# Performance work log

Measured on AMD Instinct MI355X. Metric: run time of the kernel, lower is better.

Reference implementation:

```python
import jax, jax.numpy as jnp
import numpy as np

N = 50000      # num nodes (spots)
E = 800000     # num edges before self-loops
IN = 3000      # input_dim (HVGs)
HID = 512      # hidden_dim
LAT = 30       # latent_dim
HEADS = 1
NEG_SLOPE = 0.2


def setup_inputs() -> dict:
    key = jax.random.key(0)
    ks = jax.random.split(key, 8)
    x = jax.random.normal(ks[0], (N, IN), jnp.float32)
    edge_index = jax.random.randint(ks[1], (2, E), 0, N)
    edge_attr = jax.random.uniform(ks[2], (E,), jnp.float32)
    # parameters (Xavier-ish scales)
    enc_w1 = jax.random.normal(ks[3], (HID, IN), jnp.float32) * (1.0 / np.sqrt(IN))
    enc_b1 = jnp.zeros((HID,), jnp.float32)
    gat_w = jax.random.normal(ks[4], (HID, HEADS * LAT), jnp.float32) * (1.0 / np.sqrt(HID))
    gat_att = jax.random.normal(ks[5], (HEADS, 2 * LAT), jnp.float32) * 0.1
    gat_b = jnp.zeros((LAT,), jnp.float32)
    dec_w1 = jax.random.normal(ks[6], (HID, LAT), jnp.float32) * (1.0 / np.sqrt(LAT))
    dec_b1 = jnp.zeros((HID,), jnp.float32)
    dec_b2 = jnp.zeros((IN,), jnp.float32)
    return dict(x=x, edge_index=edge_index, edge_attr=edge_attr,
                enc_w1=enc_w1, enc_b1=enc_b1, gat_w=gat_w, gat_att=gat_att,
                gat_b=gat_b, dec_w1=dec_w1, dec_b1=dec_b1, dec_b2=dec_b2)


def _gat_layer(h, src, dst, eattr, gat_w, gat_att, gat_b):
    """GAT layer: Eq.5-7, concat=False (mean over heads), multiplicative edge_attr."""
    xh = (h @ gat_w).reshape(N, HEADS, LAT)          # W h, per head
    x_i = xh[dst]                                     # target node feats (E+N, H, LAT)
    x_j = xh[src]                                     # source node feats
    att_i, att_j = gat_att[:, :LAT], gat_att[:, LAT:]
    # e_ij = LeakyReLU(a^T [Wh_i || Wh_j])
    alpha = jnp.einsum('ehc,hc->eh', x_i, att_i) + jnp.einsum('ehc,hc->eh', x_j, att_j)
    alpha = jax.nn.leaky_relu(alpha, NEG_SLOPE)
    alpha = alpha * eattr[:, None]                    # edge weight applied pre-softmax
    # segment softmax over incoming edges of each target node (self-loops ensure non-empty)
    amax = jax.ops.segment_max(alpha, dst, num_segments=N)
    alpha = jnp.exp(alpha - amax[dst])
    denom = jax.ops.segment_sum(alpha, dst, num_segments=N)
    alpha = alpha / (denom[dst] + 1e-16)
    # h'_i = sum_j alpha_ij * W h_j
    msg = x_j * alpha[:, :, None]                     # (E+N, H, LAT)
    out = jax.ops.segment_sum(msg, dst, num_segments=N)  # (N, H, LAT)
    return out.mean(axis=1) + gat_b                   # concat=False -> mean over heads


def reference(x, edge_index, edge_attr, enc_w1, enc_b1, gat_w, gat_att, gat_b,
              dec_w1, dec_b1, dec_b2):
    # add self-loops with fill_value=1.0
    loops = jnp.arange(N, dtype=edge_index.dtype)
    src = jnp.concatenate([edge_index[0], loops])
    dst = jnp.concatenate([edge_index[1], loops])
    eattr = jnp.concatenate([edge_attr, jnp.ones((N,), edge_attr.dtype)])

    # encoder: fc1 -> ELU -> GAT -> ELU
    h = jax.nn.elu(x @ enc_w1.T + enc_b1)
    z = jax.nn.elu(_gat_layer(h, src, dst, eattr, gat_w, gat_att, gat_b))

    # decoder: fc1 -> ELU -> tied fc2 (W^b = W^T, own bias)
    hd = jax.nn.elu(z @ dec_w1.T + dec_b1)
    x_recon = hd @ enc_w1 + dec_b2
    return (x_recon, z)
```

## Files before the change

kernel.cpp:

```cpp
#include <hip/hip_runtime.h>
#include <hip/hip_bf16.h>
#include <math.h>

#define N_NODES 50000
#define E_EDGES 800000
#define ET (E_EDGES + N_NODES)
#define IN_DIM 3000
#define HID 512
#define LAT 30
#define XH_STRIDE 32
#define NEG_SLOPE 0.2f
#define KPAD 3072
#define ENC_NT 94
#define APITCH 40

typedef __bf16 bfv8 __attribute__((ext_vector_type(8)));
typedef float f32x4 __attribute__((ext_vector_type(4)));

__device__ __forceinline__ float eluf(float x) { return x > 0.f ? x : expm1f(x); }

__device__ __forceinline__ unsigned fkey(float f) {
    unsigned u = __float_as_uint(f);
    return (u & 0x80000000u) ? ~u : (u | 0x80000000u);
}
__device__ __forceinline__ float funkey(unsigned k) {
    unsigned u = (k & 0x80000000u) ? (k ^ 0x80000000u) : ~k;
    return __uint_as_float(u);
}

__global__ void k_init(float* __restrict__ zbuf, unsigned* __restrict__ amax, float* __restrict__ denom) {
    int gid = blockIdx.x * 256 + threadIdx.x;
    if (gid < N_NODES * XH_STRIDE) zbuf[gid] = 0.f;
    if (gid < N_NODES) { amax[gid] = 0u; denom[gid] = 0.f; }
}

__global__ void k_transpose_w(const float* __restrict__ w, float* __restrict__ wt) {
    int idx = blockIdx.x * 256 + threadIdx.x;
    if (idx < HID * LAT) {
        int j = idx / LAT, c = idx % LAT;
        wt[c * HID + j] = w[idx];
    }
}

__global__ void k_conv_w(const float* __restrict__ w, __bf16* __restrict__ w1b, __bf16* __restrict__ w1bt) {
    int idx = blockIdx.x * 256 + threadIdx.x;
    if (idx >= HID * KPAD) return;
    int j = idx / KPAD, k = idx - j * KPAD;
    float v = (k < IN_DIM) ? w[(size_t)j * IN_DIM + k] : 0.f;
    __bf16 b = (__bf16)v;
    w1b[(size_t)j * KPAD + k] = b;
    w1bt[(size_t)k * HID + j] = b;
}

__global__ __launch_bounds__(256)
void k_enc_gemm(const float* __restrict__ A, const __bf16* __restrict__ Bb,
                const float* __restrict__ bias, float* __restrict__ C) {
    __shared__ __bf16 As[2][128 * APITCH];
    __shared__ __bf16 Bs[2][4096];
    const int tid = threadIdx.x;
    const int lane = tid & 63, wv = tid >> 6;
    const int wr = wv >> 1, wc = wv & 1;
    const int l16 = lane & 15, lh = lane >> 4;
    const int i0 = blockIdx.y * 128;
    const int c0 = blockIdx.x * 128;

    const int arow = tid >> 2, akc = tid & 3;
    const float* apA = A + (size_t)(i0 + arow) * IN_DIM + akc * 8;
    const int r1 = i0 + arow + 64;
    const float* apB = A + (size_t)(r1 < N_NODES ? r1 : N_NODES - 1) * IN_DIM + akc * 8;

    f32x4 acc[4][4] = {};
    float4 a00, a01, a10, a11;

    auto stageB = [&](int kt, int b) {
#pragma unroll
        for (int s = 0; s < 2; ++s) {
            int g = wv * 2 + s;
            int col = (g & 1) * 64 + lane, ks = g >> 1;
            const __bf16* src = Bb + (size_t)(c0 + col) * KPAD + kt + ks * 8;
            __builtin_amdgcn_global_load_lds(
                (const __attribute__((address_space(1))) void*)src,
                (__attribute__((address_space(3))) void*)(&Bs[b][(size_t)g * 512]),
                16, 0, 0);
        }
    };
    auto loadA = [&](int kt) {
        a00 = a01 = a10 = a11 = make_float4(0.f, 0.f, 0.f, 0.f);
        if (kt + akc * 8 < IN_DIM) {
            const float4* p0 = (const float4*)(apA + kt);
            a00 = p0[0]; a01 = p0[1];
            const float4* p1 = (const float4*)(apB + kt);
            a10 = p1[0]; a11 = p1[1];
        }
    };
    auto writeA = [&](int b) {
        bfv8 pk;
        pk[0] = (__bf16)a00.x; pk[1] = (__bf16)a00.y; pk[2] = (__bf16)a00.z; pk[3] = (__bf16)a00.w;
        pk[4] = (__bf16)a01.x; pk[5] = (__bf16)a01.y; pk[6] = (__bf16)a01.z; pk[7] = (__bf16)a01.w;
        *(bfv8*)&As[b][(size_t)arow * APITCH + akc * 8] = pk;
        pk[0] = (__bf16)a10.x; pk[1] = (__bf16)a10.y; pk[2] = (__bf16)a10.z; pk[3] = (__bf16)a10.w;
        pk[4] = (__bf16)a11.x; pk[5] = (__bf16)a11.y; pk[6] = (__bf16)a11.z; pk[7] = (__bf16)a11.w;
        *(bfv8*)&As[b][(size_t)(arow + 64) * APITCH + akc * 8] = pk;
    };

    stageB(0, 0);
    loadA(0);
    writeA(0);
    asm volatile("s_waitcnt vmcnt(0)" ::: "memory");
    __syncthreads();

    int cur = 0;
    for (int t = 0; t < ENC_NT; ++t) {
        bool nxt = (t + 1) < ENC_NT;
        if (nxt) {
            stageB((t + 1) * 32, cur ^ 1);
            loadA((t + 1) * 32);
        }
        bfv8 af[4], bfr[4];
#pragma unroll
        for (int mi = 0; mi < 4; ++mi)
            af[mi] = *(const bfv8*)&As[cur][(size_t)(wr * 64 + mi * 16 + l16) * APITCH + lh * 8];
#pragma unroll
        for (int ni = 0; ni < 4; ++ni)
            bfr[ni] = *(const bfv8*)&Bs[cur][((size_t)lh * 128 + wc * 64 + ni * 16 + l16) * 8];
#pragma unroll
        for (int mi = 0; mi < 4; ++mi)
#pragma unroll
            for (int ni = 0; ni < 4; ++ni)
                acc[mi][ni] = __builtin_amdgcn_mfma_f32_16x16x32_bf16(af[mi], bfr[ni], acc[mi][ni], 0, 0, 0);
        if (nxt) writeA(cur ^ 1);
        asm volatile("s_waitcnt vmcnt(0)" ::: "memory");
        __syncthreads();
        cur ^= 1;
    }

#pragma unroll
    for (int ni = 0; ni < 4; ++ni) {
        int col = c0 + wc * 64 + ni * 16 + l16;
        float bv = bias[col];
#pragma unroll
        for (int mi = 0; mi < 4; ++mi) {
            int row0 = i0 + wr * 64 + mi * 16 + lh * 4;
#pragma unroll
            for (int r = 0; r < 4; ++r) {
                int row = row0 + r;
                if (row < N_NODES)
                    C[(size_t)row * HID + col] = eluf(acc[mi][ni][r] + bv);
            }
        }
    }
}

__global__ __launch_bounds__(256)
void k_dec_gemm(const __bf16* __restrict__ Ab, const __bf16* __restrict__ Bt,
                const float* __restrict__ bias, float* __restrict__ C) {
    __shared__ __bf16 As[2][4096];
    __shared__ __bf16 Bs[2][4096];
    const int tid = threadIdx.x;
    const int lane = tid & 63, wv = tid >> 6;
    const int wr = wv >> 1, wc = wv & 1;
    const int l16 = lane & 15, lh = lane >> 4;
    const int i0 = blockIdx.y * 128;
    const int c0 = blockIdx.x * 128;

    f32x4 acc[4][4] = {};

    auto stage = [&](int kt, int b) {
#pragma unroll
        for (int s = 0; s < 2; ++s) {
            int g = wv * 2 + s;
            int rc = (g & 1) * 64 + lane, ks = g >> 1;
            int row = i0 + rc; if (row >= N_NODES) row = N_NODES - 1;
            const __bf16* srcA = Ab + (size_t)row * HID + kt + ks * 8;
            __builtin_amdgcn_global_load_lds(
                (const __attribute__((address_space(1))) void*)srcA,
                (__attribute__((address_space(3))) void*)(&As[b][(size_t)g * 512]),
                16, 0, 0);
            const __bf16* srcB = Bt + (size_t)(c0 + rc) * HID + kt + ks * 8;
            __builtin_amdgcn_global_load_lds(
                (const __attribute__((address_space(1))) void*)srcB,
                (__attribute__((address_space(3))) void*)(&Bs[b][(size_t)g * 512]),
                16, 0, 0);
        }
    };

    stage(0, 0);
    asm volatile("s_waitcnt vmcnt(0)" ::: "memory");
    __syncthreads();

    int cur = 0;
#pragma unroll 1
    for (int t = 0; t < 16; ++t) {
        if (t < 15) stage((t + 1) * 32, cur ^ 1);
        bfv8 af[4], bfr[4];
#pragma unroll
        for (int mi = 0; mi < 4; ++mi)
            af[mi] = *(const bfv8*)&As[cur][((size_t)lh * 128 + wr * 64 + mi * 16 + l16) * 8];
#pragma unroll
        for (int ni = 0; ni < 4; ++ni)
            bfr[ni] = *(const bfv8*)&Bs[cur][((size_t)lh * 128 + wc * 64 + ni * 16 + l16) * 8];
#pragma unroll
        for (int mi = 0; mi < 4; ++mi)
#pragma unroll
            for (int ni = 0; ni < 4; ++ni)
                acc[mi][ni] = __builtin_amdgcn_mfma_f32_16x16x32_bf16(af[mi], bfr[ni], acc[mi][ni], 0, 0, 0);
        asm volatile("s_waitcnt vmcnt(0)" ::: "memory");
        __syncthreads();
        cur ^= 1;
    }

#pragma unroll
    for (int ni = 0; ni < 4; ++ni) {
        int col = c0 + wc * 64 + ni * 16 + l16;
        if (col >= IN_DIM) continue;
        float bv = bias[col];
#pragma unroll
        for (int mi = 0; mi < 4; ++mi) {
            int row0 = i0 + wr * 64 + mi * 16 + lh * 4;
#pragma unroll
            for (int r = 0; r < 4; ++r) {
                int row = row0 + r;
                if (row < N_NODES)
                    C[(size_t)row * IN_DIM + col] = acc[mi][ni][r] + bv;
            }
        }
    }
}

__global__ __launch_bounds__(256)
void k_gat_proj(const float* __restrict__ h, const float* __restrict__ gat_w,
                const float* __restrict__ gat_att,
                float* __restrict__ xh, float* __restrict__ si, float* __restrict__ sj) {
    __shared__ float gwl[HID * LAT];
    __shared__ float atl[2 * LAT];
    int tid = threadIdx.x;
    for (int i = tid; i < HID * LAT; i += 256) gwl[i] = gat_w[i];
    if (tid < 2 * LAT) atl[tid] = gat_att[tid];
    __syncthreads();
    int c = tid & 31;
    bool act = c < LAT;
    for (int it = 0; it < 16; ++it) {
        int n = blockIdx.x * 128 + it * 8 + (tid >> 5);
        if (n >= N_NODES) continue;
        float accv = 0.f;
        const float4* h4 = (const float4*)(h + (size_t)n * HID);
#pragma unroll 4
        for (int j4 = 0; j4 < HID / 4; ++j4) {
            float4 hv = h4[j4];
            if (act) {
                int b = j4 * 4 * LAT + c;
                accv = fmaf(hv.x, gwl[b], accv);
                accv = fmaf(hv.y, gwl[b + LAT], accv);
                accv = fmaf(hv.z, gwl[b + 2 * LAT], accv);
                accv = fmaf(hv.w, gwl[b + 3 * LAT], accv);
            }
        }
        float xhv = act ? accv : 0.f;
        xh[(size_t)n * XH_STRIDE + c] = xhv;
        float sip = act ? atl[c] * xhv : 0.f;
        float sjp = act ? atl[LAT + c] * xhv : 0.f;
#pragma unroll
        for (int off = 16; off > 0; off >>= 1) {
            sip += __shfl_down(sip, off, 32);
            sjp += __shfl_down(sjp, off, 32);
        }
        if (c == 0) { si[n] = sip; sj[n] = sjp; }
    }
}

__global__ void k_edge_alpha(const int* __restrict__ ei, const float* __restrict__ eattr,
                             const float* __restrict__ si, const float* __restrict__ sj,
                             float* __restrict__ alphaE, unsigned* __restrict__ amax) {
    int e = blockIdx.x * 256 + threadIdx.x;
    if (e >= ET) return;
    int s, d; float w;
    if (e < E_EDGES) { s = ei[e]; d = ei[E_EDGES + e]; w = eattr[e]; }
    else { s = d = e - E_EDGES; w = 1.f; }
    float a = si[d] + sj[s];
    a = a >= 0.f ? a : NEG_SLOPE * a;
    a *= w;
    alphaE[e] = a;
    atomicMax(&amax[d], fkey(a));
}

__global__ void k_edge_exp(const int* __restrict__ ei, float* __restrict__ alphaE,
                           const unsigned* __restrict__ amax, float* __restrict__ denom) {
    int e = blockIdx.x * 256 + threadIdx.x;
    if (e >= ET) return;
    int d = (e < E_EDGES) ? ei[E_EDGES + e] : (e - E_EDGES);
    float v = expf(alphaE[e] - funkey(amax[d]));
    alphaE[e] = v;
    atomicAdd(&denom[d], v);
}

__global__ void k_edge_scatter(const int* __restrict__ ei, const float* __restrict__ alphaE,
                               const float* __restrict__ xh, float* __restrict__ zbuf) {
    int gid = blockIdx.x * 256 + threadIdx.x;
    int e = gid >> 5, c = gid & 31;
    if (e >= ET || c >= LAT) return;
    int s, d;
    if (e < E_EDGES) { s = ei[e]; d = ei[E_EDGES + e]; }
    else { s = d = e - E_EDGES; }
    atomicAdd(&zbuf[(size_t)d * XH_STRIDE + c], alphaE[e] * xh[(size_t)s * XH_STRIDE + c]);
}

__global__ void k_z(const float* __restrict__ gat_b, const float* __restrict__ denom,
                    float* __restrict__ zbuf, float* __restrict__ zout) {
    int gid = blockIdx.x * 256 + threadIdx.x;
    int n = gid >> 5, c = gid & 31;
    if (n >= N_NODES) return;
    if (c < LAT) {
        float v = eluf(zbuf[gid] / (denom[n] + 1e-16f) + gat_b[c]);
        zbuf[gid] = v;
        zout[(size_t)n * LAT + c] = v;
    }
}

__global__ __launch_bounds__(256)
void k_dec1(const float* __restrict__ zbuf, const float* __restrict__ wt,
            const float* __restrict__ b, __bf16* __restrict__ hdb) {
    int gid = blockIdx.x * 256 + threadIdx.x;
    if (gid >= N_NODES * HID) return;
    int j = gid & (HID - 1);
    size_t i = (size_t)(gid >> 9);
    float acc = b[j];
#pragma unroll
    for (int c = 0; c < LAT; ++c)
        acc = fmaf(zbuf[i * XH_STRIDE + c], wt[c * HID + j], acc);
    hdb[gid] = (__bf16)eluf(acc);
}

extern "C" void kernel_launch(void* const* d_in, const int* in_sizes, int n_in,
                              void* d_out, int out_size, void* d_ws, size_t ws_size,
                              hipStream_t stream) {
    const float* x      = (const float*)d_in[0];
    const int*   ei     = (const int*)d_in[1];
    const float* eattr  = (const float*)d_in[2];
    const float* enc_w1 = (const float*)d_in[3];
    const float* enc_b1 = (const float*)d_in[4];
    const float* gat_w  = (const float*)d_in[5];
    const float* gat_att= (const float*)d_in[6];
    const float* gat_b  = (const float*)d_in[7];
    const float* dec_w1 = (const float*)d_in[8];
    const float* dec_b1 = (const float*)d_in[9];
    const float* dec_b2 = (const float*)d_in[10];

    float* out  = (float*)d_out;
    float* xrec = out;
    float* zout = out + (size_t)N_NODES * IN_DIM;

    float* ws = (float*)d_ws;
    float*    h      = ws;
    float*    xh     = ws + 25600000;
    float*    zbuf   = ws + 27200000;
    float*    si     = ws + 28800000;
    float*    sj     = ws + 28850000;
    unsigned* amax   = (unsigned*)(ws + 28900000);
    float*    denom  = ws + 28950000;
    float*    alphaE = ws + 29000000;
    float*    wt     = ws + 29850000;
    __bf16*   w1b    = (__bf16*)(ws + 29865360);
    __bf16*   w1bt   = (__bf16*)(ws + 30651792);
    __bf16*   hdb    = (__bf16*)h;

    (void)in_sizes; (void)n_in; (void)out_size; (void)ws_size;

    k_init<<<(N_NODES * XH_STRIDE + 255) / 256, 256, 0, stream>>>(zbuf, amax, denom);
    k_transpose_w<<<(HID * LAT + 255) / 256, 256, 0, stream>>>(dec_w1, wt);
    k_conv_w<<<(HID * KPAD + 255) / 256, 256, 0, stream>>>(enc_w1, w1b, w1bt);

    {
        dim3 g(HID / 128, (N_NODES + 127) / 128);
        k_enc_gemm<<<g, 256, 0, stream>>>(x, w1b, enc_b1, h);
    }

    k_gat_proj<<<(N_NODES + 127) / 128, 256, 0, stream>>>(h, gat_w, gat_att, xh, si, sj);
    k_edge_alpha<<<(ET + 255) / 256, 256, 0, stream>>>(ei, eattr, si, sj, alphaE, amax);
    k_edge_exp<<<(ET + 255) / 256, 256, 0, stream>>>(ei, alphaE, amax, denom);
    k_edge_scatter<<<((size_t)ET * 32 + 255) / 256, 256, 0, stream>>>(ei, alphaE, xh, zbuf);
    k_z<<<(N_NODES * 32 + 255) / 256, 256, 0, stream>>>(gat_b, denom, zbuf, zout);
    k_dec1<<<(N_NODES * HID + 255) / 256, 256, 0, stream>>>(zbuf, wt, dec_b1, hdb);

    {
        dim3 g(KPAD / 128, (N_NODES + 127) / 128);
        k_dec_gemm<<<g, 256, 0, stream>>>(hdb, w1bt, dec_b2, xrec);
    }
}
```

Baseline: 1.788 ms.

## Triple-buffer GEMM B/A tiles, swizzle LDS rows, and remap block order for reuse

Both bf16 MFMA GEMMs (encoder and tied decoder) move from double to triple buffering of the global_load_lds staged tiles. They wait with partial vmcnt so two tiles stay in flight, and use raw s_barrier plus sched_barrier instead of __syncthreads. LDS rows are XOR-swizzled by the k-slice to reduce bank conflicts on fragment reads. The grid is remapped so that consecutive blocks share column tiles across groups of 8 row tiles, which is meant to improve L2 reuse. The cost is extra LDS per block, which may reduce occupancy, and correctness depends on the hand-tuned vmcnt counts.

```diff
diff --git a/kernel.cpp b/kernel.cpp
--- a/kernel.cpp
+++ b/kernel.cpp
@@ -12,6 +12,7 @@
 #define NEG_SLOPE 0.2f
 #define KPAD 3072
 #define ENC_NT 94
+#define DEC_NT 16
 #define APITCH 40
 
 typedef __bf16 bfv8 __attribute__((ext_vector_type(8)));
@@ -56,17 +57,19 @@
 void k_enc_gemm(const float* __restrict__ A, const __bf16* __restrict__ Bb,
                 const float* __restrict__ bias, float* __restrict__ C) {
     __shared__ __bf16 As[2][128 * APITCH];
-    __shared__ __bf16 Bs[2][4096];
+    __shared__ __bf16 Bs[3][4096];
     const int tid = threadIdx.x;
     const int lane = tid & 63, wv = tid >> 6;
     const int wr = wv >> 1, wc = wv & 1;
     const int l16 = lane & 15, lh = lane >> 4;
-    const int i0 = blockIdx.y * 128;
-    const int c0 = blockIdx.x * 128;
+    const int p = ((int)blockIdx.y >> 2) * 8 + (int)blockIdx.x;
+    if (p > 390) return;
+    const int i0 = p * 128;
+    const int c0 = ((int)blockIdx.y & 3) * 128;
 
     const int arow = tid >> 2, akc = tid & 3;
-    const float* apA = A + (size_t)(i0 + arow) * IN_DIM + akc * 8;
-    const int r1 = i0 + arow + 64;
+    const int r0 = i0 + arow, r1 = i0 + arow + 64;
+    const float* apA = A + (size_t)(r0 < N_NODES ? r0 : N_NODES - 1) * IN_DIM + akc * 8;
     const float* apB = A + (size_t)(r1 < N_NODES ? r1 : N_NODES - 1) * IN_DIM + akc * 8;
 
     f32x4 acc[4][4] = {};
@@ -76,7 +79,8 @@
 #pragma unroll
         for (int s = 0; s < 2; ++s) {
             int g = wv * 2 + s;
-            int col = (g & 1) * 64 + lane, ks = g >> 1;
+            int ks = g >> 1;
+            int col = (g & 1) * 64 + (lane ^ (ks << 1));
             const __bf16* src = Bb + (size_t)(c0 + col) * KPAD + kt + ks * 8;
             __builtin_amdgcn_global_load_lds(
                 (const __attribute__((address_space(1))) void*)src,
@@ -104,34 +108,41 @@
     };
 
     stageB(0, 0);
+    stageB(32, 1);
     loadA(0);
     writeA(0);
-    asm volatile("s_waitcnt vmcnt(0)" ::: "memory");
-    __syncthreads();
-
-    int cur = 0;
+    asm volatile("s_waitcnt vmcnt(0) lgkmcnt(0)" ::: "memory");
+    __builtin_amdgcn_s_barrier();
+    __builtin_amdgcn_sched_barrier(0);
+
+    int acur = 0;
     for (int t = 0; t < ENC_NT; ++t) {
-        bool nxt = (t + 1) < ENC_NT;
-        if (nxt) {
-            stageB((t + 1) * 32, cur ^ 1);
-            loadA((t + 1) * 32);
-        }
+        const int bt = t % 3;
+        const bool nxt1 = (t + 1) < ENC_NT, nxt2 = (t + 2) < ENC_NT;
+        if (nxt1) loadA((t + 1) * 32);
+        if (nxt2) stageB((t + 2) * 32, (t + 2) % 3);
+
         bfv8 af[4], bfr[4];
 #pragma unroll
         for (int mi = 0; mi < 4; ++mi)
-            af[mi] = *(const bfv8*)&As[cur][(size_t)(wr * 64 + mi * 16 + l16) * APITCH + lh * 8];
+            af[mi] = *(const bfv8*)&As[acur][(size_t)(wr * 64 + mi * 16 + l16) * APITCH + lh * 8];
 #pragma unroll
         for (int ni = 0; ni < 4; ++ni)
-            bfr[ni] = *(const bfv8*)&Bs[cur][((size_t)lh * 128 + wc * 64 + ni * 16 + l16) * 8];
+            bfr[ni] = *(const bfv8*)&Bs[bt][((size_t)lh * 128 + wc * 64 + ((ni * 16 + l16) ^ (lh << 1))) * 8];
 #pragma unroll
         for (int mi = 0; mi < 4; ++mi)
 #pragma unroll
             for (int ni = 0; ni < 4; ++ni)
                 acc[mi][ni] = __builtin_amdgcn_mfma_f32_16x16x32_bf16(af[mi], bfr[ni], acc[mi][ni], 0, 0, 0);
-        if (nxt) writeA(cur ^ 1);
-        asm volatile("s_waitcnt vmcnt(0)" ::: "memory");
-        __syncthreads();
-        cur ^= 1;
+        if (nxt1) writeA(acur ^ 1);
+        if (nxt2) {
+            asm volatile("s_waitcnt vmcnt(2) lgkmcnt(0)" ::: "memory");
+        } else {
+            asm volatile("s_waitcnt vmcnt(0) lgkmcnt(0)" ::: "memory");
+        }
+        __builtin_amdgcn_s_barrier();
+        __builtin_amdgcn_sched_barrier(0);
+        acur ^= 1;
     }
 
 #pragma unroll
@@ -154,14 +165,16 @@
 __global__ __launch_bounds__(256)
 void k_dec_gemm(const __bf16* __restrict__ Ab, const __bf16* __restrict__ Bt,
                 const float* __restrict__ bias, float* __restrict__ C) {
-    __shared__ __bf16 As[2][4096];
-    __shared__ __bf16 Bs[2][4096];
+    __shared__ __bf16 As[3][4096];
+    __shared__ __bf16 Bs[3][4096];
     const int tid = threadIdx.x;
     const int lane = tid & 63, wv = tid >> 6;
     const int wr = wv >> 1, wc = wv & 1;
     const int l16 = lane & 15, lh = lane >> 4;
-    const int i0 = blockIdx.y * 128;
-    const int c0 = blockIdx.x * 128;
+    const int p = ((int)blockIdx.y / 24) * 8 + (int)blockIdx.x;
+    if (p > 390) return;
+    const int i0 = p * 128;
+    const int c0 = ((int)blockIdx.y % 24) * 128;
 
     f32x4 acc[4][4] = {};
 
@@ -169,7 +182,8 @@
 #pragma unroll
         for (int s = 0; s < 2; ++s) {
             int g = wv * 2 + s;
-            int rc = (g & 1) * 64 + lane, ks = g >> 1;
+            int ks = g >> 1;
+            int rc = (g & 1) * 64 + (lane ^ (ks << 1));
             int row = i0 + rc; if (row >= N_NODES) row = N_NODES - 1;
             const __bf16* srcA = Ab + (size_t)row * HID + kt + ks * 8;
             __builtin_amdgcn_global_load_lds(
@@ -185,28 +199,34 @@
     };
 
     stage(0, 0);
-    asm volatile("s_waitcnt vmcnt(0)" ::: "memory");
-    __syncthreads();
-
-    int cur = 0;
+    stage(32, 1);
+    asm volatile("s_waitcnt vmcnt(4) lgkmcnt(0)" ::: "memory");
+    __builtin_amdgcn_s_barrier();
+    __builtin_amdgcn_sched_barrier(0);
+
 #pragma unroll 1
-    for (int t = 0; t < 16; ++t) {
-        if (t < 15) stage((t + 1) * 32, cur ^ 1);
+    for (int t = 0; t < DEC_NT; ++t) {
+        const int bt = t % 3;
+        if (t + 2 < DEC_NT) stage((t + 2) * 32, (t + 2) % 3);
         bfv8 af[4], bfr[4];
 #pragma unroll
         for (int mi = 0; mi < 4; ++mi)
-            af[mi] = *(const bfv8*)&As[cur][((size_t)lh * 128 + wr * 64 + mi * 16 + l16) * 8];
+            af[mi] = *(const bfv8*)&As[bt][((size_t)lh * 128 + wr * 64 + ((mi * 16 + l16) ^ (lh << 1))) * 8];
 #pragma unroll
         for (int ni = 0; ni < 4; ++ni)
-            bfr[ni] = *(const bfv8*)&Bs[cur][((size_t)lh * 128 + wc * 64 + ni * 16 + l16) * 8];
+            bfr[ni] = *(const bfv8*)&Bs[bt][((size_t)lh * 128 + wc * 64 + ((ni * 16 + l16) ^ (lh << 1))) * 8];
 #pragma unroll
         for (int mi = 0; mi < 4; ++mi)
 #pragma unroll
             for (int ni = 0; ni < 4; ++ni)
                 acc[mi][ni] = __builtin_amdgcn_mfma_f32_16x16x32_bf16(af[mi], bfr[ni], acc[mi][ni], 0, 0, 0);
-        asm volatile("s_waitcnt vmcnt(0)" ::: "memory");
-        __syncthreads();
-        cur ^= 1;
+        if (t + 2 < DEC_NT) {
+            asm volatile("s_waitcnt vmcnt(4) lgkmcnt(0)" ::: "memory");
+        } else {
+            asm volatile("s_waitcnt vmcnt(0) lgkmcnt(0)" ::: "memory");
+        }
+        __builtin_amdgcn_s_barrier();
+        __builtin_amdgcn_sched_barrier(0);
     }
 
 #pragma unroll
@@ -370,7 +390,7 @@
     k_conv_w<<<(HID * KPAD + 255) / 256, 256, 0, stream>>>(enc_w1, w1b, w1bt);
 
     {
-        dim3 g(HID / 128, (N_NODES + 127) / 128);
+        dim3 g(8, 196);
         k_enc_gemm<<<g, 256, 0, stream>>>(x, w1b, enc_b1, h);
     }
 
@@ -382,7 +402,7 @@
     k_dec1<<<(N_NODES * HID + 255) / 256, 256, 0, stream>>>(zbuf, wt, dec_b1, hdb);
 
     {
-        dim3 g(KPAD / 128, (N_NODES + 127) / 128);
+        dim3 g(8, 1176);
         k_dec_gemm<<<g, 256, 0, stream>>>(hdb, w1bt, dec_b2, xrec);
     }
 }
```

Measured after the change: 1.825 ms. 2.1% more time.
